# Kernel tuning notes

Hardware: AMD Instinct MI355X
Metric: run time of the kernel (lower is better)

The kernel has to match this reference:

```python
import jax, jax.numpy as jnp
import numpy as np

N_NODES = 100000
N_EDGES = 3200000
D_IN = 256
D_HID = 256
D_OUT = 64


def setup_inputs() -> dict:
    key = jax.random.key(0)
    k1, k2, k3, k4 = jax.random.split(key, 4)
    x = jax.random.normal(k1, (N_NODES, D_IN), dtype=jnp.float32)
    edge_index = jax.random.randint(k2, (2, N_EDGES), 0, N_NODES, dtype=jnp.int32)
    W1 = jax.random.normal(k3, (D_IN, D_HID), dtype=jnp.float32) / np.sqrt(D_IN)
    b1 = jnp.zeros((D_HID,), dtype=jnp.float32)
    W2 = jax.random.normal(k4, (D_HID, D_OUT), dtype=jnp.float32) / np.sqrt(D_HID)
    b2 = jnp.zeros((D_OUT,), dtype=jnp.float32)
    return {"x": x, "edge_index": edge_index, "W1": W1, "b1": b1, "W2": W2, "b2": b2}


def _gcn_conv(x, src, dst, norm, W, b, n_nodes):
    # dense linear transform, then normalized scatter-add aggregation
    h = x @ W  # [N, out]
    msg = norm[:, None] * h[src]  # gather + scale, [E+N, out]
    out = jax.ops.segment_sum(msg, dst, num_segments=n_nodes)
    return out + b


def reference(x, edge_index, W1, b1, W2, b2):
    n = x.shape[0]
    # add self-loops (PyG GCNConv default)
    loops = jnp.arange(n, dtype=edge_index.dtype)
    src = jnp.concatenate([edge_index[0], loops])
    dst = jnp.concatenate([edge_index[1], loops])
    # symmetric normalization deg^{-1/2}[src] * deg^{-1/2}[dst]
    deg = jax.ops.segment_sum(jnp.ones_like(src, dtype=x.dtype), dst, num_segments=n)
    dinv = jnp.where(deg > 0, jax.lax.rsqrt(jnp.maximum(deg, 1.0)), 0.0)
    norm = dinv[src] * dinv[dst]

    h = _gcn_conv(x, src, dst, norm, W1, b1, n)
    h = jax.nn.relu(h)
    # dropout is identity at inference
    h = _gcn_conv(h, src, dst, norm, W2, b2, n)
    return jax.nn.log_softmax(h, axis=1)
```

## Files before the change

### kernel.cpp

```cpp
#include <hip/hip_runtime.h>
#include <hip/hip_bf16.h>


typedef __bf16 bf16;
typedef bf16 bf16x8 __attribute__((ext_vector_type(8)));
typedef float f32x4 __attribute__((ext_vector_type(4)));
typedef float f32x2 __attribute__((ext_vector_type(2)));

#define NBLK 256

__global__ __launch_bounds__(256) void k_b1(const int* __restrict__ edge, int E, int chunk,
                                            int NB, int* __restrict__ gcnt) {
    __shared__ int cnt[512];
    int tid = threadIdx.x;
    for (int i = tid; i < NB; i += 256) cnt[i] = 0;
    __syncthreads();
    int s = blockIdx.x * chunk, e = min(s + chunk, E);
    for (int i = s + tid; i < e; i += 256) atomicAdd(&cnt[edge[E + i] >> 9], 1);
    __syncthreads();
    for (int i = tid; i < NB; i += 256) gcnt[blockIdx.x * NB + i] = cnt[i];
}

__global__ void k_b2(const int* __restrict__ gcnt, int NB, int E, int* __restrict__ bstart) {
    __shared__ int col[256];
    int k = threadIdx.x;
    int sum = 0;
    if (k < NB)
        for (int b = 0; b < NBLK; ++b) sum += gcnt[b * NB + k];
    col[k] = sum;
    __syncthreads();
    for (int o = 1; o < 256; o <<= 1) {
        int v = (k >= o) ? col[k - o] : 0;
        __syncthreads();
        col[k] += v;
        __syncthreads();
    }
    if (k < NB) bstart[k] = col[k] - sum;
    if (k == 0) bstart[NB] = E;
}

__global__ void k_b2b(int* __restrict__ gcnt, int NB, const int* __restrict__ bstart) {
    __shared__ int col[256];
    int b = threadIdx.x;
    int k = blockIdx.x;
    int v = gcnt[b * NB + k];
    col[b] = v;
    __syncthreads();
    for (int o = 1; o < 256; o <<= 1) {
        int t = (b >= o) ? col[b - o] : 0;
        __syncthreads();
        col[b] += t;
        __syncthreads();
    }
    gcnt[b * NB + k] = bstart[k] + col[b] - v;
}

__global__ __launch_bounds__(256) void k_b3(const int* __restrict__ edge, int E, int chunk,
                                            int NB, const int* __restrict__ base,
                                            int* __restrict__ ebuf) {
    __shared__ int cnt[512];
    __shared__ int bs[512];
    int tid = threadIdx.x;
    for (int i = tid; i < NB; i += 256) {
        cnt[i] = 0;
        bs[i] = base[blockIdx.x * NB + i];
    }
    __syncthreads();
    int s = blockIdx.x * chunk, e = min(s + chunk, E);
    for (int i = s + tid; i < e; i += 256) {
        int sv = edge[i], dv = edge[E + i];
        int k = dv >> 9;
        int r = atomicAdd(&cnt[k], 1);
        ebuf[bs[k] + r] = sv | ((dv & 511) << 17);
    }
}

__global__ __launch_bounds__(256) void k_b45(const int* __restrict__ ebuf,
                                             const int* __restrict__ bstart,
                                             const float* __restrict__ scale, int n, int E,
                                             int NB, int* __restrict__ off,
                                             float* __restrict__ dinv,
                                             float* __restrict__ ws) {
    __shared__ int cnt[512];
    __shared__ int red[256];
    int tid = threadIdx.x;
    int k = blockIdx.x;
    cnt[tid] = 0;
    cnt[tid + 256] = 0;
    __syncthreads();
    int s = bstart[k], e = bstart[k + 1];
    for (int i = s + tid; i < e; i += 256) atomicAdd(&cnt[(ebuf[i] >> 17) & 511], 1);
    __syncthreads();
    int c0 = cnt[tid * 2], c1 = cnt[tid * 2 + 1];
    int sum = c0 + c1;
    red[tid] = sum;
    __syncthreads();
    for (int o = 1; o < 256; o <<= 1) {
        int v = (tid >= o) ? red[tid - o] : 0;
        __syncthreads();
        red[tid] += v;
        __syncthreads();
    }
    int ex = red[tid] - sum;
    int base = k << 9;
    int g0 = base + tid * 2, g1 = g0 + 1;
    int o0 = s + ex, o1 = s + ex + c0;
    if (g0 < n) {
        off[g0] = o0;
        float d0 = rsqrtf((float)(c0 + 1));
        dinv[g0] = d0;
        ws[g0] = d0 * scale[g0];
    } else if (g0 == n) off[g0] = o0;
    if (g1 < n) {
        off[g1] = o1;
        float d1 = rsqrtf((float)(c1 + 1));
        dinv[g1] = d1;
        ws[g1] = d1 * scale[g1];
    } else if (g1 == n) off[g1] = o1;
    if (k == NB - 1 && tid == 0) off[n] = E;
}

__global__ __launch_bounds__(256) void k_b6(const int* __restrict__ ebuf,
                                            const int* __restrict__ bstart,
                                            const int* __restrict__ off,
                                            const float* __restrict__ ws, int n,
                                            int2* __restrict__ pair) {
    __shared__ int cnt[512];
    __shared__ int offl[512];
    int tid = threadIdx.x;
    int k = blockIdx.x;
    int base = k << 9;
    cnt[tid] = 0;
    cnt[tid + 256] = 0;
    offl[tid] = (base + tid < n) ? off[base + tid] : 0;
    offl[tid + 256] = (base + 256 + tid < n) ? off[base + 256 + tid] : 0;
    __syncthreads();
    int s = bstart[k], e = bstart[k + 1];
    for (int i = s + tid; i < e; i += 256) {
        int pk = ebuf[i];
        int sv = pk & 0x1ffff;
        int node = (pk >> 17) & 511;
        int r = atomicAdd(&cnt[node], 1);
        pair[offl[node] + r] = make_int2(sv << 8, __float_as_int(ws[sv]));
    }
}

__global__ __launch_bounds__(256) void k_quant(const float* __restrict__ x,
                                               unsigned char* __restrict__ xqA,
                                               unsigned char* __restrict__ xqB,
                                               float* __restrict__ scale, int n) {
    int row = blockIdx.x * 4 + (threadIdx.x >> 6);
    int lane = threadIdx.x & 63;
    if (row >= n) return;
    f32x4 v = ((const f32x4*)x)[(size_t)row * 64 + lane];
    float m = fmaxf(fmaxf(fabsf(v[0]), fabsf(v[1])), fmaxf(fabsf(v[2]), fabsf(v[3])));
    for (int o = 32; o > 0; o >>= 1) m = fmaxf(m, __shfl_xor(m, o));
    m = fmaxf(m, 1e-20f);
    float inv = 127.0f / m;
    int b0 = (__float2int_rn(v[0] * inv) + 128) & 255;
    int b1 = (__float2int_rn(v[1] * inv) + 128) & 255;
    int b2 = (__float2int_rn(v[2] * inv) + 128) & 255;
    int b3 = (__float2int_rn(v[3] * inv) + 128) & 255;
    int word = b0 | (b1 << 8) | (b2 << 16) | (b3 << 24);
    if (lane < 32) ((int*)xqA)[(size_t)row * 32 + lane] = word;
    else           ((int*)xqB)[(size_t)row * 32 + (lane - 32)] = word;
    if (lane == 0) scale[row] = m / 127.0f;
}

__global__ void k_wt(const float* __restrict__ W1, const float* __restrict__ W2,
                     bf16* __restrict__ W1t, bf16* __restrict__ W2t) {
    int b = blockIdx.x;
    int k = threadIdx.x;
    if (b < 256) W1t[b * 256 + k] = (bf16)W1[k * 256 + b];
    else { int nc = b - 256; W2t[nc * 256 + k] = (bf16)W2[k * 64 + nc]; }
}

__device__ __forceinline__ void acc16(f32x2 a[8], uint4 t, float w, float& wsum) {
    wsum += w;
    f32x2 w2 = {w, w};
    unsigned u0 = t.x, u1 = t.y, u2 = t.z, u3 = t.w;
    f32x2 c;
    c[0] = (float)(u0 & 255u);         c[1] = (float)((u0 >> 8) & 255u);  a[0] += w2 * c;
    c[0] = (float)((u0 >> 16) & 255u); c[1] = (float)(u0 >> 24);         a[1] += w2 * c;
    c[0] = (float)(u1 & 255u);         c[1] = (float)((u1 >> 8) & 255u);  a[2] += w2 * c;
    c[0] = (float)((u1 >> 16) & 255u); c[1] = (float)(u1 >> 24);         a[3] += w2 * c;
    c[0] = (float)(u2 & 255u);         c[1] = (float)((u2 >> 8) & 255u);  a[4] += w2 * c;
    c[0] = (float)((u2 >> 16) & 255u); c[1] = (float)(u2 >> 24);         a[5] += w2 * c;
    c[0] = (float)(u3 & 255u);         c[1] = (float)((u3 >> 8) & 255u);  a[6] += w2 * c;
    c[0] = (float)((u3 >> 16) & 255u); c[1] = (float)(u3 >> 24);         a[7] += w2 * c;
}

__device__ __forceinline__ void acc8(f32x2 a[4], int2 t, float w, float& wsum) {
    wsum += w;
    f32x2 w2 = {w, w};
    unsigned u0 = (unsigned)t.x, u1 = (unsigned)t.y;
    f32x2 c;
    c[0] = (float)(u0 & 255u);         c[1] = (float)((u0 >> 8) & 255u);  a[0] += w2 * c;
    c[0] = (float)((u0 >> 16) & 255u); c[1] = (float)(u0 >> 24);         a[1] += w2 * c;
    c[0] = (float)(u1 & 255u);         c[1] = (float)((u1 >> 8) & 255u);  a[2] += w2 * c;
    c[0] = (float)((u1 >> 16) & 255u); c[1] = (float)(u1 >> 24);         a[3] += w2 * c;
}

__global__ __launch_bounds__(256) void k_agg1h(const unsigned char* __restrict__ xqh,
                                               const float* __restrict__ wsv,
                                               const int* __restrict__ off,
                                               const int2* __restrict__ pair,
                                               const float* __restrict__ dinv,
                                               bf16* __restrict__ ax, int hofs, int n) {
    int wv = blockIdx.x * 4 + (threadIdx.x >> 6);
    int lane = threadIdx.x & 63;
    int node = wv * 8 + (lane >> 3);
    int l8 = lane & 7;
    if (node >= n) return;
    int s0 = off[node], s1 = off[node + 1];
    float dv = dinv[node];
    const unsigned char* xqb = xqh + l8 * 16;
    f32x2 a[8] = {};
    float wsum = 0.0f;
    uint4 xs = *(const uint4*)(xqb + (size_t)node * 128);
    acc16(a, xs, wsv[node], wsum);
    int e = s0;
    if (s1 - s0 >= 8) {
        int2 p[8];
#pragma unroll
        for (int q = 0; q < 8; ++q) p[q] = pair[s0 + q];
        e = s0 + 8;
        for (; e + 8 <= s1; e += 8) {
            uint4 t[8];
#pragma unroll
            for (int q = 0; q < 8; ++q)
                t[q] = *(const uint4*)(xqb + ((unsigned)p[q].x >> 1));
            int2 pn[8];
#pragma unroll
            for (int q = 0; q < 8; ++q) pn[q] = pair[e + q];
#pragma unroll
            for (int q = 0; q < 8; ++q) acc16(a, t[q], __int_as_float(p[q].y), wsum);
#pragma unroll
            for (int q = 0; q < 8; ++q) p[q] = pn[q];
        }
        uint4 t[8];
#pragma unroll
        for (int q = 0; q < 8; ++q)
            t[q] = *(const uint4*)(xqb + ((unsigned)p[q].x >> 1));
#pragma unroll
        for (int q = 0; q < 8; ++q) acc16(a, t[q], __int_as_float(p[q].y), wsum);
    }
    for (; e < s1; ++e) {
        int2 p = pair[e];
        uint4 t = *(const uint4*)(xqb + ((unsigned)p.x >> 1));
        acc16(a, t, __int_as_float(p.y), wsum);
    }
    float c = 128.0f * wsum;
    bf16x8 o0, o1;
#pragma unroll
    for (int j = 0; j < 4; ++j) {
        o0[2 * j]     = (bf16)((a[j][0] - c) * dv);
        o0[2 * j + 1] = (bf16)((a[j][1] - c) * dv);
        o1[2 * j]     = (bf16)((a[4 + j][0] - c) * dv);
        o1[2 * j + 1] = (bf16)((a[4 + j][1] - c) * dv);
    }
    ((bf16x8*)ax)[(size_t)node * 32 + hofs + l8 * 2] = o0;
    ((bf16x8*)ax)[(size_t)node * 32 + hofs + l8 * 2 + 1] = o1;
}

__device__ __forceinline__ int swz(int s) { return s ^ ((s >> 3) & 7); }

__global__ __launch_bounds__(512) void k_gemmp(const bf16* __restrict__ A,
                                               const bf16* __restrict__ Bt,
                                               const float* __restrict__ bias,
                                               bf16* __restrict__ C, int n) {
    __shared__ __align__(16) bf16 As[8 * 64 * 8];
    __shared__ __align__(16) bf16 Bs[16 * 64 * 8];
    int tid = threadIdx.x;
    int bm = blockIdx.x * 128;
    int w = tid >> 6, lane = tid & 63;
    int wm = w >> 2;
    int wn = w & 3;

    int r = tid >> 2;
    int cq = tid & 3;
    int a_slot = swz(((r >> 4) * 64) + cq * 16 + (r & 15));
    int arow = bm + r; if (arow > n - 1) arow = n - 1;

    f32x4 acc[4][4] = {};

    for (int k0 = 0; k0 < 256; k0 += 32) {
        __syncthreads();
        uint4 av = *(const uint4*)(A + (size_t)arow * 256 + k0 + cq * 8);
        *(uint4*)(As + a_slot * 8) = av;
#pragma unroll
        for (int rep = 0; rep < 2; ++rep) {
            int r2 = rep * 128 + r;
            uint4 bv = *(const uint4*)(Bt + (size_t)r2 * 256 + k0 + cq * 8);
            *(uint4*)(Bs + swz(((r2 >> 4) * 64) + cq * 16 + (r2 & 15)) * 8) = bv;
        }
        __syncthreads();
        bf16x8 af[4], bfr[4];
#pragma unroll
        for (int i = 0; i < 4; ++i)
            af[i] = *(const bf16x8*)(As + swz(((wm * 4 + i) * 64) + lane) * 8);
#pragma unroll
        for (int j = 0; j < 4; ++j)
            bfr[j] = *(const bf16x8*)(Bs + swz(((wn * 4 + j) * 64) + lane) * 8);
#pragma unroll
        for (int i = 0; i < 4; ++i)
#pragma unroll
            for (int j = 0; j < 4; ++j)
                acc[i][j] = __builtin_amdgcn_mfma_f32_16x16x32_bf16(af[i], bfr[j], acc[i][j], 0, 0, 0);
    }

    int colb = lane & 15, rowq = lane >> 4;
#pragma unroll
    for (int i = 0; i < 4; ++i)
#pragma unroll
        for (int j = 0; j < 4; ++j) {
            int col = wn * 64 + j * 16 + colb;
            float bv = bias[col];
#pragma unroll
            for (int rr = 0; rr < 4; ++rr) {
                int row = bm + wm * 64 + i * 16 + rowq * 4 + rr;
                if (row < n) {
                    float v = acc[i][j][rr] + bv;
                    C[(size_t)row * 256 + col] = (bf16)(v > 0.0f ? v : 0.0f);
                }
            }
        }
}

__global__ __launch_bounds__(256) void k_gemm2q(const bf16* __restrict__ A,
                                                const bf16* __restrict__ Bt,
                                                const float* __restrict__ dinv,
                                                unsigned char* __restrict__ tq,
                                                float* __restrict__ w2v, int n) {
    __shared__ __align__(16) bf16 As[4 * 64 * 8];
    __shared__ __align__(16) bf16 Bs[4 * 64 * 8];
    __shared__ float tbf[64][65];
    int tid = threadIdx.x;
    int bm = blockIdx.x * 64;
    int w = tid >> 6, lane = tid & 63;
    int wm = w >> 1, wn = w & 1;

    int r = tid >> 2;
    int cq = tid & 3;
    int lds_slot = swz(((r >> 4) * 64) + cq * 16 + (r & 15));
    int arow = bm + r; if (arow > n - 1) arow = n - 1;

    f32x4 acc[2][2] = {};

    for (int k0 = 0; k0 < 256; k0 += 32) {
        __syncthreads();
        uint4 av = *(const uint4*)(A + (size_t)arow * 256 + k0 + cq * 8);
        uint4 bv = *(const uint4*)(Bt + (size_t)r * 256 + k0 + cq * 8);
        *(uint4*)(As + lds_slot * 8) = av;
        *(uint4*)(Bs + lds_slot * 8) = bv;
        __syncthreads();
#pragma unroll
        for (int i = 0; i < 2; ++i) {
            bf16x8 af = *(const bf16x8*)(As + swz((wm * 2 + i) * 64 + lane) * 8);
#pragma unroll
            for (int j = 0; j < 2; ++j) {
                bf16x8 bfr = *(const bf16x8*)(Bs + swz((wn * 2 + j) * 64 + lane) * 8);
                acc[i][j] = __builtin_amdgcn_mfma_f32_16x16x32_bf16(af, bfr, acc[i][j], 0, 0, 0);
            }
        }
    }

    int colb = lane & 15, rowq = lane >> 4;
    __syncthreads();
#pragma unroll
    for (int i = 0; i < 2; ++i)
#pragma unroll
        for (int j = 0; j < 2; ++j)
#pragma unroll
            for (int rr = 0; rr < 4; ++rr)
                tbf[wm * 32 + i * 16 + rowq * 4 + rr][wn * 32 + j * 16 + colb] = acc[i][j][rr];
    __syncthreads();

    int row = tid >> 2, l4 = tid & 3;
    int grow = bm + row;
    if (grow < n) {
        float f[16], m = 0.0f;
#pragma unroll
        for (int k = 0; k < 16; ++k) { f[k] = tbf[row][l4 * 16 + k]; m = fmaxf(m, fabsf(f[k])); }
        m = fmaxf(m, __shfl_xor(m, 1));
        m = fmaxf(m, __shfl_xor(m, 2));
        m = fmaxf(m, 1e-20f);
        float inv = 127.0f / m;
        int wd[4];
#pragma unroll
        for (int g = 0; g < 4; ++g) {
            int acc_w = 0;
#pragma unroll
            for (int b = 0; b < 4; ++b)
                acc_w |= ((__float2int_rn(f[g * 4 + b] * inv) + 128) & 255) << (8 * b);
            wd[g] = acc_w;
        }
        ((int4*)tq)[(size_t)grow * 4 + l4] = make_int4(wd[0], wd[1], wd[2], wd[3]);
        if (l4 == 0) w2v[grow] = dinv[grow] * (m / 127.0f);
    }
}

__global__ __launch_bounds__(256) void k_agg2(const unsigned char* __restrict__ tq,
                                              const float* __restrict__ w2v,
                                              const int* __restrict__ off,
                                              const int2* __restrict__ pair,
                                              const float* __restrict__ dinv,
                                              const float* __restrict__ b2,
                                              float* __restrict__ out, int n) {
    int wv = blockIdx.x * 4 + (threadIdx.x >> 6);
    int lane = threadIdx.x & 63;
    int node = wv * 8 + (lane >> 3);
    int l8 = lane & 7;
    if (node >= n) return;
    int s0 = off[node], s1 = off[node + 1];
    float dv = dinv[node];
    const unsigned char* tqb = tq + l8 * 8;
    int2 ts = *(const int2*)(tqb + (size_t)node * 64);
    f32x2 a[4] = {};
    float wsum = 0.0f;
    acc8(a, ts, w2v[node], wsum);
    int e = s0;
    if (s1 - s0 >= 8) {
        int2 p[8]; float sc[8];
#pragma unroll
        for (int q = 0; q < 8; ++q) p[q] = pair[s0 + q];
#pragma unroll
        for (int q = 0; q < 8; ++q) sc[q] = w2v[(unsigned)p[q].x >> 8];
        e = s0 + 8;
        for (; e + 8 <= s1; e += 8) {
            int2 t[8];
#pragma unroll
            for (int q = 0; q < 8; ++q) t[q] = *(const int2*)(tqb + ((unsigned)p[q].x >> 2));
            int2 pn[8];
#pragma unroll
            for (int q = 0; q < 8; ++q) pn[q] = pair[e + q];
            float scn[8];
#pragma unroll
            for (int q = 0; q < 8; ++q) scn[q] = w2v[(unsigned)pn[q].x >> 8];
#pragma unroll
            for (int q = 0; q < 8; ++q) acc8(a, t[q], sc[q], wsum);
#pragma unroll
            for (int q = 0; q < 8; ++q) { p[q] = pn[q]; sc[q] = scn[q]; }
        }
        int2 t[8];
#pragma unroll
        for (int q = 0; q < 8; ++q) t[q] = *(const int2*)(tqb + ((unsigned)p[q].x >> 2));
#pragma unroll
        for (int q = 0; q < 8; ++q) acc8(a, t[q], sc[q], wsum);
    }
    for (; e < s1; ++e) {
        int2 p = pair[e];
        float w = w2v[(unsigned)p.x >> 8];
        int2 t = *(const int2*)(tqb + ((unsigned)p.x >> 2));
        acc8(a, t, w, wsum);
    }
    float c = 128.0f * wsum;
    float aa[8];
#pragma unroll
    for (int j = 0; j < 4; ++j) { aa[2 * j] = a[j][0]; aa[2 * j + 1] = a[j][1]; }
    const float4* B2 = (const float4*)b2;
    float4 bv0 = B2[l8 * 2], bv1 = B2[l8 * 2 + 1];
    aa[0] = (aa[0] - c) * dv + bv0.x; aa[1] = (aa[1] - c) * dv + bv0.y;
    aa[2] = (aa[2] - c) * dv + bv0.z; aa[3] = (aa[3] - c) * dv + bv0.w;
    aa[4] = (aa[4] - c) * dv + bv1.x; aa[5] = (aa[5] - c) * dv + bv1.y;
    aa[6] = (aa[6] - c) * dv + bv1.z; aa[7] = (aa[7] - c) * dv + bv1.w;
    float m = aa[0];
#pragma unroll
    for (int j = 1; j < 8; ++j) m = fmaxf(m, aa[j]);
    for (int o = 4; o > 0; o >>= 1) m = fmaxf(m, __shfl_xor(m, o));
    float s = 0.0f;
#pragma unroll
    for (int j = 0; j < 8; ++j) s += __expf(aa[j] - m);
    for (int o = 4; o > 0; o >>= 1) s += __shfl_xor(s, o);
    float ls = m + __logf(s);
    f32x4 o0, o1;
    o0[0] = aa[0] - ls; o0[1] = aa[1] - ls; o0[2] = aa[2] - ls; o0[3] = aa[3] - ls;
    o1[0] = aa[4] - ls; o1[1] = aa[5] - ls; o1[2] = aa[6] - ls; o1[3] = aa[7] - ls;
    f32x4* O = (f32x4*)out;
    O[(size_t)node * 16 + l8 * 2] = o0;
    O[(size_t)node * 16 + l8 * 2 + 1] = o1;
}

extern "C" void kernel_launch(void* const* d_in, const int* in_sizes, int n_in,
                              void* d_out, int out_size, void* d_ws, size_t ws_size,
                              hipStream_t stream) {
    const float* x   = (const float*)d_in[0];
    const int*  edge = (const int*)d_in[1];
    const float* W1  = (const float*)d_in[2];
    const float* b1  = (const float*)d_in[3];
    const float* W2  = (const float*)d_in[4];
    const float* b2  = (const float*)d_in[5];
    float* out = (float*)d_out;

    int n = in_sizes[0] / 256;
    int E = in_sizes[1] / 2;
    int NB = (n + 511) >> 9;
    int chunk = (E + NBLK - 1) / NBLK;

    char* ws = (char*)d_ws;
    auto alloc = [&](size_t bytes) -> char* {
        char* p = ws;
        ws += (bytes + 255) & ~(size_t)255;
        return p;
    };
    int*   gcnt   = (int*)alloc((size_t)NBLK * NB * 4);
    int*   bstart = (int*)alloc((size_t)(NB + 1) * 4);
    int*   ebuf   = (int*)alloc((size_t)E * 4);
    float* dinv   = (float*)alloc((size_t)n * 4);
    float* wsv    = (float*)alloc((size_t)n * 4);
    int*   off    = (int*)alloc((size_t)(n + 1) * 4);
    int2*  pair   = (int2*)alloc((size_t)E * 8);
    unsigned char* xqA = (unsigned char*)alloc((size_t)n * 128);
    unsigned char* xqB = (unsigned char*)alloc((size_t)n * 128);
    float* scale  = (float*)alloc((size_t)n * 4);
    bf16*  ax     = (bf16*)alloc((size_t)n * 256 * 2);
    bf16*  h1     = (bf16*)alloc((size_t)n * 256 * 2);
    unsigned char* tq = (unsigned char*)alloc((size_t)n * 64);
    float* w2v    = (float*)alloc((size_t)n * 4);
    bf16*  W1t    = (bf16*)alloc(256 * 256 * 2);
    bf16*  W2t    = (bf16*)alloc(64 * 256 * 2);

    k_quant<<<(n + 3) / 4, 256, 0, stream>>>(x, xqA, xqB, scale, n);

    k_b1<<<NBLK, 256, 0, stream>>>(edge, E, chunk, NB, gcnt);
    k_b2<<<1, 256, 0, stream>>>(gcnt, NB, E, bstart);
    k_b2b<<<NB, 256, 0, stream>>>(gcnt, NB, bstart);
    k_b3<<<NBLK, 256, 0, stream>>>(edge, E, chunk, NB, gcnt, ebuf);
    k_b45<<<NB, 256, 0, stream>>>(ebuf, bstart, scale, n, E, NB, off, dinv, wsv);
    k_b6<<<NB, 256, 0, stream>>>(ebuf, bstart, off, wsv, n, pair);

    k_wt<<<320, 256, 0, stream>>>(W1, W2, W1t, W2t);

    k_agg1h<<<(n + 31) / 32, 256, 0, stream>>>(xqA, wsv, off, pair, dinv, ax, 0, n);
    k_agg1h<<<(n + 31) / 32, 256, 0, stream>>>(xqB, wsv, off, pair, dinv, ax, 16, n);
    k_gemmp<<<(n + 127) / 128, 512, 0, stream>>>(ax, W1t, b1, h1, n);

    k_gemm2q<<<(n + 63) / 64, 256, 0, stream>>>(h1, W2t, dinv, tq, w2v, n);
    k_agg2<<<(n + 31) / 32, 256, 0, stream>>>(tq, w2v, off, pair, dinv, b2, out, n);
}
```

Before: 526.2 us.

## Fuse prep kernels and aggregate full-width quantized rows in a single pass

Merges the quantize, bucket-count and weight-transpose kernels into one launch that branches on block index. The layer-1 aggregation now reads full 256-byte int8 rows in one pass with 16 lanes per node, instead of two half-width passes over split buffers. This removes launch overhead and a second traversal of the edge pair list, at the cost of larger gathers per edge (which may hurt cache locality) and fewer nodes per wave.

```diff
diff --git a/kernel.cpp b/kernel.cpp
--- a/kernel.cpp
+++ b/kernel.cpp
@@ -9,16 +9,46 @@
 
 #define NBLK 256
 
-__global__ __launch_bounds__(256) void k_b1(const int* __restrict__ edge, int E, int chunk,
-                                            int NB, int* __restrict__ gcnt) {
-    __shared__ int cnt[512];
+__global__ __launch_bounds__(256) void k_prep(const float* __restrict__ x,
+                                              unsigned char* __restrict__ xq,
+                                              float* __restrict__ scale, int n, int nqb,
+                                              const int* __restrict__ edge, int E, int chunk,
+                                              int NB, int* __restrict__ gcnt,
+                                              const float* __restrict__ W1,
+                                              const float* __restrict__ W2,
+                                              bf16* __restrict__ W1t,
+                                              bf16* __restrict__ W2t) {
+    int b = blockIdx.x;
     int tid = threadIdx.x;
-    for (int i = tid; i < NB; i += 256) cnt[i] = 0;
-    __syncthreads();
-    int s = blockIdx.x * chunk, e = min(s + chunk, E);
-    for (int i = s + tid; i < e; i += 256) atomicAdd(&cnt[edge[E + i] >> 9], 1);
-    __syncthreads();
-    for (int i = tid; i < NB; i += 256) gcnt[blockIdx.x * NB + i] = cnt[i];
+    if (b < nqb) {
+        int row = b * 4 + (tid >> 6);
+        int lane = tid & 63;
+        if (row >= n) return;
+        f32x4 v = ((const f32x4*)x)[(size_t)row * 64 + lane];
+        float m = fmaxf(fmaxf(fabsf(v[0]), fabsf(v[1])), fmaxf(fabsf(v[2]), fabsf(v[3])));
+        for (int o = 32; o > 0; o >>= 1) m = fmaxf(m, __shfl_xor(m, o));
+        m = fmaxf(m, 1e-20f);
+        float inv = 127.0f / m;
+        int b0 = (__float2int_rn(v[0] * inv) + 128) & 255;
+        int b1v = (__float2int_rn(v[1] * inv) + 128) & 255;
+        int b2v = (__float2int_rn(v[2] * inv) + 128) & 255;
+        int b3v = (__float2int_rn(v[3] * inv) + 128) & 255;
+        ((int*)xq)[(size_t)row * 64 + lane] = b0 | (b1v << 8) | (b2v << 16) | (b3v << 24);
+        if (lane == 0) scale[row] = m / 127.0f;
+    } else if (b < nqb + NBLK) {
+        int blk = b - nqb;
+        __shared__ int cnt[512];
+        for (int i = tid; i < NB; i += 256) cnt[i] = 0;
+        __syncthreads();
+        int s = blk * chunk, e = min(s + chunk, E);
+        for (int i = s + tid; i < e; i += 256) atomicAdd(&cnt[edge[E + i] >> 9], 1);
+        __syncthreads();
+        for (int i = tid; i < NB; i += 256) gcnt[blk * NB + i] = cnt[i];
+    } else {
+        int bb = b - nqb - NBLK;
+        if (bb < 256) W1t[bb * 256 + tid] = (bf16)W1[tid * 256 + bb];
+        else { int nc = bb - 256; W2t[nc * 256 + tid] = (bf16)W2[tid * 64 + nc]; }
+    }
 }
 
 __global__ void k_b2(const int* __restrict__ gcnt, int NB, int E, int* __restrict__ bstart) {
@@ -145,36 +175,6 @@
     }
 }
 
-__global__ __launch_bounds__(256) void k_quant(const float* __restrict__ x,
-                                               unsigned char* __restrict__ xqA,
-                                               unsigned char* __restrict__ xqB,
-                                               float* __restrict__ scale, int n) {
-    int row = blockIdx.x * 4 + (threadIdx.x >> 6);
-    int lane = threadIdx.x & 63;
-    if (row >= n) return;
-    f32x4 v = ((const f32x4*)x)[(size_t)row * 64 + lane];
-    float m = fmaxf(fmaxf(fabsf(v[0]), fabsf(v[1])), fmaxf(fabsf(v[2]), fabsf(v[3])));
-    for (int o = 32; o > 0; o >>= 1) m = fmaxf(m, __shfl_xor(m, o));
-    m = fmaxf(m, 1e-20f);
-    float inv = 127.0f / m;
-    int b0 = (__float2int_rn(v[0] * inv) + 128) & 255;
-    int b1 = (__float2int_rn(v[1] * inv) + 128) & 255;
-    int b2 = (__float2int_rn(v[2] * inv) + 128) & 255;
-    int b3 = (__float2int_rn(v[3] * inv) + 128) & 255;
-    int word = b0 | (b1 << 8) | (b2 << 16) | (b3 << 24);
-    if (lane < 32) ((int*)xqA)[(size_t)row * 32 + lane] = word;
-    else           ((int*)xqB)[(size_t)row * 32 + (lane - 32)] = word;
-    if (lane == 0) scale[row] = m / 127.0f;
-}
-
-__global__ void k_wt(const float* __restrict__ W1, const float* __restrict__ W2,
-                     bf16* __restrict__ W1t, bf16* __restrict__ W2t) {
-    int b = blockIdx.x;
-    int k = threadIdx.x;
-    if (b < 256) W1t[b * 256 + k] = (bf16)W1[k * 256 + b];
-    else { int nc = b - 256; W2t[nc * 256 + k] = (bf16)W2[k * 64 + nc]; }
-}
-
 __device__ __forceinline__ void acc16(f32x2 a[8], uint4 t, float w, float& wsum) {
     wsum += w;
     f32x2 w2 = {w, w};
@@ -201,23 +201,23 @@
     c[0] = (float)((u1 >> 16) & 255u); c[1] = (float)(u1 >> 24);         a[3] += w2 * c;
 }
 
-__global__ __launch_bounds__(256) void k_agg1h(const unsigned char* __restrict__ xqh,
-                                               const float* __restrict__ wsv,
-                                               const int* __restrict__ off,
-                                               const int2* __restrict__ pair,
-                                               const float* __restrict__ dinv,
-                                               bf16* __restrict__ ax, int hofs, int n) {
+__global__ __launch_bounds__(256) void k_agg1(const unsigned char* __restrict__ xq,
+                                              const float* __restrict__ wsv,
+                                              const int* __restrict__ off,
+                                              const int2* __restrict__ pair,
+                                              const float* __restrict__ dinv,
+                                              bf16* __restrict__ ax, int n) {
     int wv = blockIdx.x * 4 + (threadIdx.x >> 6);
     int lane = threadIdx.x & 63;
-    int node = wv * 8 + (lane >> 3);
-    int l8 = lane & 7;
+    int node = wv * 4 + (lane >> 4);
+    int l16 = lane & 15;
     if (node >= n) return;
     int s0 = off[node], s1 = off[node + 1];
     float dv = dinv[node];
-    const unsigned char* xqb = xqh + l8 * 16;
+    const unsigned char* xqb = xq + l16 * 16;
     f32x2 a[8] = {};
     float wsum = 0.0f;
-    uint4 xs = *(const uint4*)(xqb + (size_t)node * 128);
+    uint4 xs = *(const uint4*)(xqb + (size_t)node * 256);
     acc16(a, xs, wsv[node], wsum);
     int e = s0;
     if (s1 - s0 >= 8) {
@@ -229,7 +229,7 @@
             uint4 t[8];
 #pragma unroll
             for (int q = 0; q < 8; ++q)
-                t[q] = *(const uint4*)(xqb + ((unsigned)p[q].x >> 1));
+                t[q] = *(const uint4*)(xqb + (unsigned)p[q].x);
             int2 pn[8];
 #pragma unroll
             for (int q = 0; q < 8; ++q) pn[q] = pair[e + q];
@@ -241,13 +241,13 @@
         uint4 t[8];
 #pragma unroll
         for (int q = 0; q < 8; ++q)
-            t[q] = *(const uint4*)(xqb + ((unsigned)p[q].x >> 1));
+            t[q] = *(const uint4*)(xqb + (unsigned)p[q].x);
 #pragma unroll
         for (int q = 0; q < 8; ++q) acc16(a, t[q], __int_as_float(p[q].y), wsum);
     }
     for (; e < s1; ++e) {
         int2 p = pair[e];
-        uint4 t = *(const uint4*)(xqb + ((unsigned)p.x >> 1));
+        uint4 t = *(const uint4*)(xqb + (unsigned)p.x);
         acc16(a, t, __int_as_float(p.y), wsum);
     }
     float c = 128.0f * wsum;
@@ -259,8 +259,8 @@
         o1[2 * j]     = (bf16)((a[4 + j][0] - c) * dv);
         o1[2 * j + 1] = (bf16)((a[4 + j][1] - c) * dv);
     }
-    ((bf16x8*)ax)[(size_t)node * 32 + hofs + l8 * 2] = o0;
-    ((bf16x8*)ax)[(size_t)node * 32 + hofs + l8 * 2 + 1] = o1;
+    ((bf16x8*)ax)[(size_t)node * 32 + l16 * 2] = o0;
+    ((bf16x8*)ax)[(size_t)node * 32 + l16 * 2 + 1] = o1;
 }
 
 __device__ __forceinline__ int swz(int s) { return s ^ ((s >> 3) & 7); }
@@ -510,8 +510,7 @@
     float* wsv    = (float*)alloc((size_t)n * 4);
     int*   off    = (int*)alloc((size_t)(n + 1) * 4);
     int2*  pair   = (int2*)alloc((size_t)E * 8);
-    unsigned char* xqA = (unsigned char*)alloc((size_t)n * 128);
-    unsigned char* xqB = (unsigned char*)alloc((size_t)n * 128);
+    unsigned char* xq = (unsigned char*)alloc((size_t)n * 256);
     float* scale  = (float*)alloc((size_t)n * 4);
     bf16*  ax     = (bf16*)alloc((size_t)n * 256 * 2);
     bf16*  h1     = (bf16*)alloc((size_t)n * 256 * 2);
@@ -520,19 +519,18 @@
     bf16*  W1t    = (bf16*)alloc(256 * 256 * 2);
     bf16*  W2t    = (bf16*)alloc(64 * 256 * 2);
 
-    k_quant<<<(n + 3) / 4, 256, 0, stream>>>(x, xqA, xqB, scale, n);
-
-    k_b1<<<NBLK, 256, 0, stream>>>(edge, E, chunk, NB, gcnt);
+    int nqb = (n + 3) / 4;
+    k_prep<<<nqb + NBLK + 320, 256, 0, stream>>>(x, xq, scale, n, nqb,
+                                                 edge, E, chunk, NB, gcnt,
+                                                 W1, W2, W1t, W2t);
+
     k_b2<<<1, 256, 0, stream>>>(gcnt, NB, E, bstart);
     k_b2b<<<NB, 256, 0, stream>>>(gcnt, NB, bstart);
     k_b3<<<NBLK, 256, 0, stream>>>(edge, E, chunk, NB, gcnt, ebuf);
     k_b45<<<NB, 256, 0, stream>>>(ebuf, bstart, scale, n, E, NB, off, dinv, wsv);
     k_b6<<<NB, 256, 0, stream>>>(ebuf, bstart, off, wsv, n, pair);
 
-    k_wt<<<320, 256, 0, stream>>>(W1, W2, W1t, W2t);
-
-    k_agg1h<<<(n + 31) / 32, 256, 0, stream>>>(xqA, wsv, off, pair, dinv, ax, 0, n);
-    k_agg1h<<<(n + 31) / 32, 256, 0, stream>>>(xqB, wsv, off, pair, dinv, ax, 16, n);
+    k_agg1<<<(n + 15) / 16, 256, 0, stream>>>(xq, wsv, off, pair, dinv, ax, n);
     k_gemmp<<<(n + 127) / 128, 512, 0, stream>>>(ax, W1t, b1, h1, n);
 
     k_gemm2q<<<(n + 63) / 64, 256, 0, stream>>>(h1, W2t, dinv, tq, w2v, n);
```

Measured after the change: 515.0 us. -2.1%, faster.
